# Optimization experiments

Hardware: AMD Instinct MI355X
Metric: run time of the kernel (lower is better)

The kernel has to match this reference:

```python
import jax, jax.numpy as jnp
import numpy as np

N = 50000   # n_nodes
E = 500000  # n_edges
D = 128     # input_dim == hidden_dim
L = 2       # n_layers
K = 5       # Chebyshev filter size


def setup_inputs() -> dict:
    key = jax.random.key(0)
    k0, k1, k2, k3, k4 = jax.random.split(key, 5)
    scale = 1.0 / np.sqrt(D)
    return {
        "edge_index": jax.random.randint(k0, (2, E), 0, N),
        "edge_weight": jax.random.uniform(k1, (E,), dtype=jnp.float32),
        "emb": jax.random.uniform(k2, (N, D), dtype=jnp.float32, minval=-1.0, maxval=1.0),
        "Wx": jax.random.normal(k3, (L, 3, K, D, D), dtype=jnp.float32) * scale,
        "bx": jnp.zeros((L, 3, D), dtype=jnp.float32),
        "Wh": jax.random.normal(k4, (L, 3, K, D, D), dtype=jnp.float32) * scale,
        "bh": jnp.zeros((L, 3, D), dtype=jnp.float32),
    }


def reference(edge_index, edge_weight, emb, Wx, bx, Wh, bh):
    src, dst = edge_index[0], edge_index[1]
    # ChebConv sym-normalized scaled Laplacian with lambda_max=2:
    # L_hat = L - I = -D^{-1/2} A D^{-1/2} (zero diagonal)
    deg = jax.ops.segment_sum(edge_weight, src, num_segments=N)
    dinv = jnp.where(deg > 0, deg ** -0.5, 0.0)
    w = -dinv[src] * edge_weight * dinv[dst]  # [E]

    def prop(x):  # L_hat @ x via gather/scatter over edges
        return jax.ops.segment_sum(w[:, None] * x[src], dst, num_segments=N)

    def cheb(x, W, b):  # sum_k T_k(L_hat) x W_k + b
        Tx0 = x
        out = Tx0 @ W[0]
        Tx1 = prop(Tx0)
        out = out + Tx1 @ W[1]
        for k in range(2, K):
            Tx2 = 2.0 * prop(Tx1) - Tx0
            out = out + Tx2 @ W[k]
            Tx0, Tx1 = Tx1, Tx2
        return out + b

    x = emb
    hidden_states = []
    for l in range(L):
        H = jnp.ones((N, D), x.dtype)  # init__hidd: ones
        Z = jax.nn.sigmoid(cheb(x, Wx[l, 0], bx[l, 0]) + cheb(H, Wh[l, 0], bh[l, 0]))
        R = jax.nn.sigmoid(cheb(x, Wx[l, 1], bx[l, 1]) + cheb(H, Wh[l, 1], bh[l, 1]))
        Ht = jnp.tanh(cheb(x, Wx[l, 2], bx[l, 2]) + cheb(H * R, Wh[l, 2], bh[l, 2]))
        Hn = Z * H + (1.0 - Z) * Ht
        h = jax.nn.relu(Hn)  # dropout is identity in eval mode
        hidden_states.append(h)
        x = h
    return x  # == hidden_states[-1]
```

## Files before the change

kernel.cpp:

```cpp
#include <hip/hip_runtime.h>
#include <math.h>

#define NN 50000
#define EE 500000
#define DD 128
#define KK 5
#define LL 2

typedef _Float16 f16x8 __attribute__((ext_vector_type(8)));
typedef float f32x4 __attribute__((ext_vector_type(4)));

__device__ __forceinline__ ushort f2h(float x) {
    union { _Float16 h; ushort u; } v; v.h = (_Float16)x; return v.u;
}


__global__ __launch_bounds__(256) void edge_pass1(
    const int* __restrict__ src, const int* __restrict__ dst,
    const float* __restrict__ ew,
    float* __restrict__ deg, int* __restrict__ hist)
{
    int e = blockIdx.x * blockDim.x + threadIdx.x;
    if (e >= EE) return;
    atomicAdd(&deg[src[e]], ew[e]);
    atomicAdd(&hist[dst[e]], 1);
}

__global__ __launch_bounds__(256) void dinv_kernel(
    const float* __restrict__ deg, float* __restrict__ dinv)
{
    int i = blockIdx.x * blockDim.x + threadIdx.x;
    if (i >= NN) return;
    float d = deg[i];
    dinv[i] = (d > 0.f) ? (1.f / sqrtf(d)) : 0.f;
}

#define SCAN_C ((NN + 1023) / 1024)
__global__ __launch_bounds__(1024) void scan_kernel(
    const int* __restrict__ hist, int* __restrict__ row_ptr)
{
    __shared__ int sums[1024];
    const int t = threadIdx.x;
    const int base = t * SCAN_C;
    int local[SCAN_C];
    int s = 0;
#pragma unroll
    for (int j = 0; j < SCAN_C; ++j) {
        int i = base + j;
        int v = (i < NN) ? hist[i] : 0;
        s += v;
        local[j] = s;
    }
    sums[t] = s;
    __syncthreads();
    for (int off = 1; off < 1024; off <<= 1) {
        int v = (t >= off) ? sums[t - off] : 0;
        __syncthreads();
        sums[t] += v;
        __syncthreads();
    }
    int excl = sums[t] - s;
    if (t == 0) row_ptr[0] = 0;
#pragma unroll
    for (int j = 0; j < SCAN_C; ++j) {
        int i = base + j;
        if (i < NN) row_ptr[i + 1] = excl + local[j];
    }
}

__global__ __launch_bounds__(256) void copy_fill(
    const int* __restrict__ row_ptr, int* __restrict__ fill)
{
    int i = blockIdx.x * blockDim.x + threadIdx.x;
    if (i < NN) fill[i] = row_ptr[i];
}

__global__ __launch_bounds__(256) void edge_scatter(
    const int* __restrict__ src, const int* __restrict__ dst,
    const float* __restrict__ ew, const float* __restrict__ dinv,
    int* __restrict__ fill,
    int* __restrict__ src_srt, float* __restrict__ w_srt)
{
    int e = blockIdx.x * blockDim.x + threadIdx.x;
    if (e >= EE) return;
    int s = src[e], t = dst[e];
    float w = -dinv[s] * ew[e] * dinv[t];
    int pos = atomicAdd(&fill[t], 1);
    src_srt[pos] = s;
    w_srt[pos] = w;
}

__global__ __launch_bounds__(256) void propv_kernel(
    const int* __restrict__ rp, const int* __restrict__ ss, const float* __restrict__ sw,
    const float* __restrict__ tin, const float* __restrict__ tprev, float* __restrict__ tout,
    float alpha, float beta, int ones_in, int ones_prev)
{
    int i = blockIdx.x * blockDim.x + threadIdx.x;
    if (i >= NN) return;
    float acc = 0.f;
    int e0 = rp[i], e1 = rp[i + 1];
    int e = e0;
    for (; e + 4 <= e1; e += 4) {
        float t0 = ones_in ? 1.f : tin[ss[e]];
        float t1v = ones_in ? 1.f : tin[ss[e + 1]];
        float t2v = ones_in ? 1.f : tin[ss[e + 2]];
        float t3v = ones_in ? 1.f : tin[ss[e + 3]];
        acc += sw[e] * t0 + sw[e + 1] * t1v + sw[e + 2] * t2v + sw[e + 3] * t3v;
    }
    for (; e < e1; ++e) {
        float tv = ones_in ? 1.f : tin[ss[e]];
        acc += sw[e] * tv;
    }
    float pv = ones_prev ? 1.f : (tprev ? tprev[i] : 0.f);
    tout[i] = alpha * acc + beta * pv;
}

__global__ __launch_bounds__(128) void colsum_kernel(
    const float* __restrict__ Wh, float* __restrict__ scol)
{
    int b = blockIdx.x;
    int k = b % KK;
    int g = (b / KK) % 2;
    int l = b / (2 * KK);
    int d = threadIdx.x;
    const float* Wp = Wh + ((size_t)((l * 3 + g) * KK + k)) * DD * DD;
    float s = 0.f;
    for (int r = 0; r < DD; ++r) s += Wp[r * DD + d];
    scol[((size_t)((l * 2 + g) * KK + k)) * DD + d] = s;
}

__global__ __launch_bounds__(256) void wconv_f16(
    const float* __restrict__ W, ushort* __restrict__ out, int mode)
{
    int t = blockIdx.x;
    int st = (mode == 0) ? t : ((t / KK) * 3 + 2) * KK + (t % KK);
    const float* Wp = W + (size_t)st * DD * DD;
    ushort* op = out + (size_t)t * DD * DD;
    for (int idx = threadIdx.x; idx < DD * DD; idx += 256) {
        int rb = idx >> 7, c = idx & 127;
        float w = Wp[c * DD + rb];
        int byte = rb * 256 + (((c * 2) ^ ((rb & 7) << 4)));
        *(ushort*)((char*)op + byte) = f2h(w);
    }
}

__global__ __launch_bounds__(256) void f32_to_f16(
    const float* __restrict__ in, ushort* __restrict__ out, int n8)
{
    int i = blockIdx.x * blockDim.x + threadIdx.x;
    if (i >= n8) return;
    float4 a = ((const float4*)in)[i * 2];
    float4 b = ((const float4*)in)[i * 2 + 1];
    f16x8 o;
    o[0] = (_Float16)a.x; o[1] = (_Float16)a.y; o[2] = (_Float16)a.z; o[3] = (_Float16)a.w;
    o[4] = (_Float16)b.x; o[5] = (_Float16)b.y; o[6] = (_Float16)b.z; o[7] = (_Float16)b.w;
    ((f16x8*)out)[i] = o;
}

__global__ __launch_bounds__(256) void prop_mat(
    const int* __restrict__ rp, const int* __restrict__ ss, const float* __restrict__ sw,
    const ushort* __restrict__ x, const ushort* __restrict__ prev,
    ushort* __restrict__ out, float alpha, float beta)
{
    int node = blockIdx.x * 16 + (threadIdx.x >> 4);
    if (node >= NN) return;
    int lane = threadIdx.x & 15;
    int c = lane * 8;
    float acc[8];
#pragma unroll
    for (int j = 0; j < 8; ++j) acc[j] = 0.f;
    int e0 = rp[node], e1 = rp[node + 1];
    int e = e0;
    for (; e + 4 <= e1; e += 4) {
        int s0 = ss[e], s1 = ss[e + 1], s2 = ss[e + 2], s3 = ss[e + 3];
        float w0 = sw[e], w1 = sw[e + 1], w2 = sw[e + 2], w3 = sw[e + 3];
        f16x8 r0 = *(const f16x8*)(x + (size_t)s0 * DD + c);
        f16x8 r1 = *(const f16x8*)(x + (size_t)s1 * DD + c);
        f16x8 r2 = *(const f16x8*)(x + (size_t)s2 * DD + c);
        f16x8 r3 = *(const f16x8*)(x + (size_t)s3 * DD + c);
#pragma unroll
        for (int j = 0; j < 8; ++j)
            acc[j] += w0 * (float)r0[j] + w1 * (float)r1[j] + w2 * (float)r2[j] + w3 * (float)r3[j];
    }
    for (; e < e1; ++e) {
        int s = ss[e];
        float w = sw[e];
        f16x8 r = *(const f16x8*)(x + (size_t)s * DD + c);
#pragma unroll
        for (int j = 0; j < 8; ++j) acc[j] += w * (float)r[j];
    }
    f16x8 o;
    if (beta != 0.f && prev) {
        f16x8 pv = *(const f16x8*)(prev + (size_t)node * DD + c);
#pragma unroll
        for (int j = 0; j < 8; ++j) o[j] = (_Float16)(alpha * acc[j] + beta * (float)pv[j]);
    } else {
#pragma unroll
        for (int j = 0; j < 8; ++j) o[j] = (_Float16)(alpha * acc[j]);
    }
    *(f16x8*)(out + (size_t)node * DD + c) = o;
}

__device__ __forceinline__ void mm_gate(
    const ushort* __restrict__ const* Ts, const ushort* __restrict__ Wg,
    ushort* Bs, int rowg0, int rowg1, bool ok0, bool ok1,
    int tid, int lk, f32x4 acc[2][8], int lr)
{
#pragma unroll
    for (int fr = 0; fr < 2; ++fr)
#pragma unroll
        for (int fc = 0; fc < 8; ++fc) acc[fr][fc] = (f32x4){0.f, 0.f, 0.f, 0.f};
#pragma unroll
    for (int k = 0; k < KK; ++k) {
        const ushort* Tk = Ts[k];
        const ushort* Bg = Wg + (size_t)k * (DD * DD);
        __syncthreads();
#pragma unroll
        for (int i = 0; i < 8; ++i) {
            int off = i * 4096 + tid * 16;
            uint4 v = *(const uint4*)((const char*)Bg + off);
            *(uint4*)((char*)Bs + off) = v;
        }
        f16x8 a[2][4];
#pragma unroll
        for (int fr = 0; fr < 2; ++fr) {
            int rowg = fr ? rowg1 : rowg0;
            bool ok = fr ? ok1 : ok0;
            const ushort* rp2 = Ts[k] + (size_t)rowg * DD + lk * 8;
            (void)Tk;
#pragma unroll
            for (int ko = 0; ko < 4; ++ko) {
                if (ok) a[fr][ko] = *(const f16x8*)(rp2 + ko * 32);
                else a[fr][ko] = (f16x8){0, 0, 0, 0, 0, 0, 0, 0};
            }
        }
        __syncthreads();
#pragma unroll
        for (int ko = 0; ko < 4; ++ko) {
            const int cb = ko * 64 + lk * 16;
#pragma unroll
            for (int fc = 0; fc < 8; ++fc) {
                int rb = fc * 16 + lr;
                int byte = (rb * 256 + cb) ^ ((rb & 7) << 4);
                f16x8 bfrag = *(const f16x8*)((const char*)Bs + byte);
                acc[0][fc] = __builtin_amdgcn_mfma_f32_16x16x32_f16(a[0][ko], bfrag, acc[0][fc], 0, 0, 0);
                acc[1][fc] = __builtin_amdgcn_mfma_f32_16x16x32_f16(a[1][ko], bfrag, acc[1][fc], 0, 0, 0);
            }
        }
    }
}

__device__ __forceinline__ int xcd_swz(int b, int nwg) {
    int xcd = b & 7, idx = b >> 3;
    int q = nwg >> 3, rr = nwg & 7;
    int start = (xcd < rr) ? xcd * (q + 1) : rr * (q + 1) + (xcd - rr) * q;
    return start + idx;
}

__global__ __launch_bounds__(256) void cheb_mm_zr(
    const ushort* __restrict__ T0, const ushort* __restrict__ T1,
    const ushort* __restrict__ T2, const ushort* __restrict__ T3,
    const ushort* __restrict__ T4,
    const ushort* __restrict__ Wt,
    const float* __restrict__ tvec, const float* __restrict__ scol,
    const float* __restrict__ bx, const float* __restrict__ bh, int l,
    float* __restrict__ Xz, ushort* __restrict__ Xr16, float* __restrict__ Xh)
{
    __shared__ ushort Bs[DD * DD];
    const int tile = xcd_swz(blockIdx.x, gridDim.x);
    const int tid = threadIdx.x;
    const int lane = tid & 63;
    const int wid = tid >> 6;
    const int lr = lane & 15;
    const int lk = lane >> 4;
    const int r0 = tile * 128;
    const ushort* Ts[5] = {T0, T1, T2, T3, T4};

    int rowg0 = r0 + wid * 32 + lr;
    int rowg1 = rowg0 + 16;
    bool ok0 = rowg0 < NN;
    bool ok1 = rowg1 < NN;

    f32x4 accZ[2][8], accB[2][8];
    mm_gate(Ts, Wt, Bs, rowg0, rowg1, ok0, ok1, tid, lk, accZ, lr);
    mm_gate(Ts, Wt + (size_t)KK * DD * DD, Bs, rowg0, rowg1, ok0, ok1, tid, lk, accB, lr);

    {
        const float* s0 = scol + (size_t)((l * 2 + 0) * KK) * DD;
        const float* s1 = scol + (size_t)((l * 2 + 1) * KK) * DD;
        const float* bz0 = bx + (size_t)(l * 3 + 0) * DD;
        const float* bz1 = bh + (size_t)(l * 3 + 0) * DD;
        const float* br0 = bx + (size_t)(l * 3 + 1) * DD;
        const float* br1 = bh + (size_t)(l * 3 + 1) * DD;
#pragma unroll
        for (int fr = 0; fr < 2; ++fr) {
#pragma unroll
            for (int j = 0; j < 4; ++j) {
                int grow = r0 + wid * 32 + fr * 16 + lk * 4 + j;
                if (grow < NN) {
                    float t1 = tvec[grow], t2 = tvec[NN + grow];
                    float t3 = tvec[2 * NN + grow], t4 = tvec[3 * NN + grow];
#pragma unroll
                    for (int fc = 0; fc < 8; ++fc) {
                        int d = fc * 16 + lr;
                        size_t idx = (size_t)grow * DD + d;
                        float hz = s0[d] + t1 * s0[DD + d] + t2 * s0[2 * DD + d]
                                 + t3 * s0[3 * DD + d] + t4 * s0[4 * DD + d];
                        float z = accZ[fr][fc][j] + bz0[d] + bz1[d] + hz;
                        z = 1.f / (1.f + expf(-z));
                        float hr = s1[d] + t1 * s1[DD + d] + t2 * s1[2 * DD + d]
                                 + t3 * s1[3 * DD + d] + t4 * s1[4 * DD + d];
                        float r = accB[fr][fc][j] + br0[d] + br1[d] + hr;
                        r = 1.f / (1.f + expf(-r));
                        Xz[idx] = z;
                        Xr16[idx] = f2h(r);
                    }
                }
            }
        }
    }

    mm_gate(Ts, Wt + (size_t)2 * KK * DD * DD, Bs, rowg0, rowg1, ok0, ok1, tid, lk, accZ, lr);
#pragma unroll
    for (int fr = 0; fr < 2; ++fr) {
#pragma unroll
        for (int j = 0; j < 4; ++j) {
            int grow = r0 + wid * 32 + fr * 16 + lk * 4 + j;
            if (grow < NN) {
#pragma unroll
                for (int fc = 0; fc < 8; ++fc) {
                    int d = fc * 16 + lr;
                    Xh[(size_t)grow * DD + d] = accZ[fr][fc][j];
                }
            }
        }
    }
}

__global__ __launch_bounds__(256) void cheb_mm_final(
    const ushort* __restrict__ T0, const ushort* __restrict__ T1,
    const ushort* __restrict__ T2, const ushort* __restrict__ T3,
    const ushort* __restrict__ T4,
    const ushort* __restrict__ Wt,
    const float* __restrict__ Xh, const float* __restrict__ Xz,
    const float* __restrict__ bx, const float* __restrict__ bh, int l,
    float* __restrict__ out, ushort* __restrict__ h16, int write_f32)
{
    __shared__ ushort Bs[DD * DD];
    const int tile = xcd_swz(blockIdx.x, gridDim.x);
    const int tid = threadIdx.x;
    const int lane = tid & 63;
    const int wid = tid >> 6;
    const int lr = lane & 15;
    const int lk = lane >> 4;
    const int r0 = tile * 128;
    const ushort* Ts[5] = {T0, T1, T2, T3, T4};

    int rowg0 = r0 + wid * 32 + lr;
    int rowg1 = rowg0 + 16;
    bool ok0 = rowg0 < NN;
    bool ok1 = rowg1 < NN;

    f32x4 acc[2][8];
    mm_gate(Ts, Wt, Bs, rowg0, rowg1, ok0, ok1, tid, lk, acc, lr);

    const float* b0 = bx + (size_t)(l * 3 + 2) * DD;
    const float* b1 = bh + (size_t)(l * 3 + 2) * DD;
#pragma unroll
    for (int fr = 0; fr < 2; ++fr) {
#pragma unroll
        for (int j = 0; j < 4; ++j) {
            int grow = r0 + wid * 32 + fr * 16 + lk * 4 + j;
            if (grow < NN) {
#pragma unroll
                for (int fc = 0; fc < 8; ++fc) {
                    int d = fc * 16 + lr;
                    size_t idx = (size_t)grow * DD + d;
                    float pre = acc[fr][fc][j] + Xh[idx] + b0[d] + b1[d];
                    float ht = tanhf(pre);
                    float z = Xz[idx];
                    float hn = z + (1.f - z) * ht;
                    float h = hn > 0.f ? hn : 0.f;
                    if (write_f32) out[idx] = h;
                    h16[idx] = f2h(h);
                }
            }
        }
    }
}


extern "C" void kernel_launch(void* const* d_in, const int* in_sizes, int n_in,
                              void* d_out, int out_size, void* d_ws, size_t ws_size,
                              hipStream_t stream)
{
    const int*   ei  = (const int*)d_in[0];
    const float* ew  = (const float*)d_in[1];
    const float* emb = (const float*)d_in[2];
    const float* Wx  = (const float*)d_in[3];
    const float* bx  = (const float*)d_in[4];
    const float* Wh  = (const float*)d_in[5];
    const float* bh  = (const float*)d_in[6];
    float* out = (float*)d_out;

    const int* src = ei;
    const int* dst = ei + EE;

    char* ws = (char*)d_ws;
    size_t off = 0;
    auto alloc = [&](size_t nbytes) -> char* {
        char* p = ws + off;
        off = (off + nbytes + 255) & ~(size_t)255;
        return p;
    };
    float*  deg     = (float*)alloc((size_t)NN * 4);
    float*  dinv    = (float*)alloc((size_t)NN * 4);
    int*    hist    = (int*)alloc((size_t)(NN + 1) * 4);
    int*    row_ptr = (int*)alloc((size_t)(NN + 1) * 4);
    int*    fill    = (int*)alloc((size_t)(NN + 1) * 4);
    int*    src_srt = (int*)alloc((size_t)EE * 4);
    float*  w_srt   = (float*)alloc((size_t)EE * 4);
    float*  tvec    = (float*)alloc((size_t)4 * NN * 4);
    float*  scol    = (float*)alloc((size_t)LL * 2 * KK * DD * 4);
    float*  Xz      = (float*)alloc((size_t)NN * DD * 4);
    float*  Xh      = (float*)alloc((size_t)NN * DD * 4);
    ushort* Th      = (ushort*)alloc((size_t)4 * NN * DD * 2);
    ushort* x_f16   = (ushort*)alloc((size_t)NN * DD * 2);
    ushort* Xr_f16  = (ushort*)alloc((size_t)NN * DD * 2);
    ushort* WxT     = (ushort*)alloc((size_t)LL * 3 * KK * DD * DD * 2);
    ushort* WhT2    = (ushort*)alloc((size_t)LL * KK * DD * DD * 2);
    (void)ws_size; (void)in_sizes; (void)n_in; (void)out_size;

    ushort* T1 = Th;
    ushort* T2 = Th + (size_t)NN * DD;
    ushort* T3 = Th + (size_t)2 * NN * DD;
    ushort* T4 = Th + (size_t)3 * NN * DD;

    const int EG = (EE + 255) / 256;
    const int NG = (NN + 255) / 256;
    const int PG = (NN + 15) / 16;
    const int MMG = (NN + 127) / 128;
    const int CVG = (NN * DD / 8 + 255) / 256;
    const int GATE_STRIDE = KK * DD * DD;

    hipMemsetAsync(deg, 0, (size_t)NN * 4, stream);
    hipMemsetAsync(hist, 0, (size_t)(NN + 1) * 4, stream);

    edge_pass1<<<EG, 256, 0, stream>>>(src, dst, ew, deg, hist);
    dinv_kernel<<<NG, 256, 0, stream>>>(deg, dinv);
    scan_kernel<<<1, 1024, 0, stream>>>(hist, row_ptr);
    copy_fill<<<NG, 256, 0, stream>>>(row_ptr, fill);
    edge_scatter<<<EG, 256, 0, stream>>>(src, dst, ew, dinv, fill, src_srt, w_srt);

    float* t1 = tvec;
    float* t2 = tvec + NN;
    float* t3 = tvec + 2 * NN;
    float* t4 = tvec + 3 * NN;
    propv_kernel<<<NG, 256, 0, stream>>>(row_ptr, src_srt, w_srt, nullptr, nullptr, t1, 1.f,  0.f, 1, 0);
    propv_kernel<<<NG, 256, 0, stream>>>(row_ptr, src_srt, w_srt, t1, nullptr,      t2, 2.f, -1.f, 0, 1);
    propv_kernel<<<NG, 256, 0, stream>>>(row_ptr, src_srt, w_srt, t2, t1,           t3, 2.f, -1.f, 0, 0);
    propv_kernel<<<NG, 256, 0, stream>>>(row_ptr, src_srt, w_srt, t3, t2,           t4, 2.f, -1.f, 0, 0);

    colsum_kernel<<<LL * 2 * KK, 128, 0, stream>>>(Wh, scol);

    wconv_f16<<<LL * 3 * KK, 256, 0, stream>>>(Wx, WxT, 0);
    wconv_f16<<<LL * KK, 256, 0, stream>>>(Wh, WhT2, 1);

    f32_to_f16<<<CVG, 256, 0, stream>>>(emb, x_f16, NN * DD / 8);

    for (int l = 0; l < LL; ++l) {
        prop_mat<<<PG, 256, 0, stream>>>(row_ptr, src_srt, w_srt, x_f16, nullptr, T1, 1.f,  0.f);
        prop_mat<<<PG, 256, 0, stream>>>(row_ptr, src_srt, w_srt, T1,    x_f16,   T2, 2.f, -1.f);
        prop_mat<<<PG, 256, 0, stream>>>(row_ptr, src_srt, w_srt, T2,    T1,      T3, 2.f, -1.f);
        prop_mat<<<PG, 256, 0, stream>>>(row_ptr, src_srt, w_srt, T3,    T2,      T4, 2.f, -1.f);

        cheb_mm_zr<<<MMG, 256, 0, stream>>>(x_f16, T1, T2, T3, T4,
                                            WxT + (size_t)l * 3 * GATE_STRIDE,
                                            tvec, scol, bx, bh, l,
                                            Xz, Xr_f16, Xh);

        prop_mat<<<PG, 256, 0, stream>>>(row_ptr, src_srt, w_srt, Xr_f16, nullptr, T1, 1.f,  0.f);
        prop_mat<<<PG, 256, 0, stream>>>(row_ptr, src_srt, w_srt, T1,     Xr_f16,  T2, 2.f, -1.f);
        prop_mat<<<PG, 256, 0, stream>>>(row_ptr, src_srt, w_srt, T2,     T1,      T3, 2.f, -1.f);
        prop_mat<<<PG, 256, 0, stream>>>(row_ptr, src_srt, w_srt, T3,     T2,      T4, 2.f, -1.f);

        cheb_mm_final<<<MMG, 256, 0, stream>>>(Xr_f16, T1, T2, T3, T4,
                                               WhT2 + (size_t)l * GATE_STRIDE,
                                               Xh, Xz, bx, bh, l,
                                               out, x_f16, (l == LL - 1) ? 1 : 0);
    }
}
```

Baseline: 957.5 us.

## Split gate matmuls across blocks, prelayout weights as MFMA fragments, widen gather unroll

The combined Z/R/H matmul kernel is split so each block computes one gate, tripling the grid. The final matmul uses 64-row tiles to launch more blocks. Weights are pre-laid out in MFMA fragment order, so the B operand becomes a single contiguous LDS read per lane instead of swizzled addressing. The sparse propagation gets an 8-way unrolled edge loop with nontemporal index and output accesses, and the last layer skips its redundant f16 store. In exchange, the T-matrix rows are reloaded once per gate, and each block now does less work per weight tile it stages.

Result: faster. 898.7 us (-6.1%).

```diff
diff --git a/kernel.cpp b/kernel.cpp
--- a/kernel.cpp
+++ b/kernel.cpp
@@ -9,6 +9,7 @@
 
 typedef _Float16 f16x8 __attribute__((ext_vector_type(8)));
 typedef float f32x4 __attribute__((ext_vector_type(4)));
+typedef unsigned int u32x4 __attribute__((ext_vector_type(4)));
 
 __device__ __forceinline__ ushort f2h(float x) {
     union { _Float16 h; ushort u; } v; v.h = (_Float16)x; return v.u;
@@ -129,7 +130,7 @@
     scol[((size_t)((l * 2 + g) * KK + k)) * DD + d] = s;
 }
 
-__global__ __launch_bounds__(256) void wconv_f16(
+__global__ __launch_bounds__(256) void wconv_frag(
     const float* __restrict__ W, ushort* __restrict__ out, int mode)
 {
     int t = blockIdx.x;
@@ -137,10 +138,14 @@
     const float* Wp = W + (size_t)st * DD * DD;
     ushort* op = out + (size_t)t * DD * DD;
     for (int idx = threadIdx.x; idx < DD * DD; idx += 256) {
-        int rb = idx >> 7, c = idx & 127;
-        float w = Wp[c * DD + rb];
-        int byte = rb * 256 + (((c * 2) ^ ((rb & 7) << 4)));
-        *(ushort*)((char*)op + byte) = f2h(w);
+        int j  = idx & 7;
+        int lr = (idx >> 3) & 15;
+        int lk = (idx >> 7) & 3;
+        int fc = (idx >> 9) & 7;
+        int ko = (idx >> 12) & 3;
+        int dout = fc * 16 + lr;
+        int din  = ko * 32 + lk * 8 + j;
+        op[idx] = f2h(Wp[din * DD + dout]);
     }
 }
 
@@ -171,6 +176,36 @@
     for (int j = 0; j < 8; ++j) acc[j] = 0.f;
     int e0 = rp[node], e1 = rp[node + 1];
     int e = e0;
+    for (; e + 8 <= e1; e += 8) {
+        int s0 = __builtin_nontemporal_load(ss + e);
+        int s1 = __builtin_nontemporal_load(ss + e + 1);
+        int s2 = __builtin_nontemporal_load(ss + e + 2);
+        int s3 = __builtin_nontemporal_load(ss + e + 3);
+        int s4 = __builtin_nontemporal_load(ss + e + 4);
+        int s5 = __builtin_nontemporal_load(ss + e + 5);
+        int s6 = __builtin_nontemporal_load(ss + e + 6);
+        int s7 = __builtin_nontemporal_load(ss + e + 7);
+        float w0 = __builtin_nontemporal_load(sw + e);
+        float w1 = __builtin_nontemporal_load(sw + e + 1);
+        float w2 = __builtin_nontemporal_load(sw + e + 2);
+        float w3 = __builtin_nontemporal_load(sw + e + 3);
+        float w4 = __builtin_nontemporal_load(sw + e + 4);
+        float w5 = __builtin_nontemporal_load(sw + e + 5);
+        float w6 = __builtin_nontemporal_load(sw + e + 6);
+        float w7 = __builtin_nontemporal_load(sw + e + 7);
+        f16x8 r0 = *(const f16x8*)(x + (size_t)s0 * DD + c);
+        f16x8 r1 = *(const f16x8*)(x + (size_t)s1 * DD + c);
+        f16x8 r2 = *(const f16x8*)(x + (size_t)s2 * DD + c);
+        f16x8 r3 = *(const f16x8*)(x + (size_t)s3 * DD + c);
+        f16x8 r4 = *(const f16x8*)(x + (size_t)s4 * DD + c);
+        f16x8 r5 = *(const f16x8*)(x + (size_t)s5 * DD + c);
+        f16x8 r6 = *(const f16x8*)(x + (size_t)s6 * DD + c);
+        f16x8 r7 = *(const f16x8*)(x + (size_t)s7 * DD + c);
+#pragma unroll
+        for (int j = 0; j < 8; ++j)
+            acc[j] += w0 * (float)r0[j] + w1 * (float)r1[j] + w2 * (float)r2[j] + w3 * (float)r3[j]
+                    + w4 * (float)r4[j] + w5 * (float)r5[j] + w6 * (float)r6[j] + w7 * (float)r7[j];
+    }
     for (; e + 4 <= e1; e += 4) {
         int s0 = ss[e], s1 = ss[e + 1], s2 = ss[e + 2], s3 = ss[e + 3];
         float w0 = sw[e], w1 = sw[e + 1], w2 = sw[e + 2], w3 = sw[e + 3];
@@ -189,30 +224,30 @@
 #pragma unroll
         for (int j = 0; j < 8; ++j) acc[j] += w * (float)r[j];
     }
-    f16x8 o;
+    union { f16x8 v; u32x4 u; } o;
     if (beta != 0.f && prev) {
         f16x8 pv = *(const f16x8*)(prev + (size_t)node * DD + c);
 #pragma unroll
-        for (int j = 0; j < 8; ++j) o[j] = (_Float16)(alpha * acc[j] + beta * (float)pv[j]);
+        for (int j = 0; j < 8; ++j) o.v[j] = (_Float16)(alpha * acc[j] + beta * (float)pv[j]);
     } else {
 #pragma unroll
-        for (int j = 0; j < 8; ++j) o[j] = (_Float16)(alpha * acc[j]);
-    }
-    *(f16x8*)(out + (size_t)node * DD + c) = o;
-}
-
+        for (int j = 0; j < 8; ++j) o.v[j] = (_Float16)(alpha * acc[j]);
+    }
+    __builtin_nontemporal_store(o.u, (u32x4*)(out + (size_t)node * DD + c));
+}
+
+template<int NFR>
 __device__ __forceinline__ void mm_gate(
     const ushort* __restrict__ const* Ts, const ushort* __restrict__ Wg,
-    ushort* Bs, int rowg0, int rowg1, bool ok0, bool ok1,
-    int tid, int lk, f32x4 acc[2][8], int lr)
-{
-#pragma unroll
-    for (int fr = 0; fr < 2; ++fr)
+    ushort* Bs, const int* rowg, const bool* ok,
+    int tid, int lane, int lk, f32x4 acc[NFR][8])
+{
+#pragma unroll
+    for (int fr = 0; fr < NFR; ++fr)
 #pragma unroll
         for (int fc = 0; fc < 8; ++fc) acc[fr][fc] = (f32x4){0.f, 0.f, 0.f, 0.f};
 #pragma unroll
     for (int k = 0; k < KK; ++k) {
-        const ushort* Tk = Ts[k];
         const ushort* Bg = Wg + (size_t)k * (DD * DD);
         __syncthreads();
 #pragma unroll
@@ -221,30 +256,25 @@
             uint4 v = *(const uint4*)((const char*)Bg + off);
             *(uint4*)((char*)Bs + off) = v;
         }
-        f16x8 a[2][4];
-#pragma unroll
-        for (int fr = 0; fr < 2; ++fr) {
-            int rowg = fr ? rowg1 : rowg0;
-            bool ok = fr ? ok1 : ok0;
-            const ushort* rp2 = Ts[k] + (size_t)rowg * DD + lk * 8;
-            (void)Tk;
+        f16x8 a[NFR][4];
+#pragma unroll
+        for (int fr = 0; fr < NFR; ++fr) {
+            const ushort* rp2 = Ts[k] + (size_t)rowg[fr] * DD + lk * 8;
 #pragma unroll
             for (int ko = 0; ko < 4; ++ko) {
-                if (ok) a[fr][ko] = *(const f16x8*)(rp2 + ko * 32);
+                if (ok[fr]) a[fr][ko] = *(const f16x8*)(rp2 + ko * 32);
                 else a[fr][ko] = (f16x8){0, 0, 0, 0, 0, 0, 0, 0};
             }
         }
         __syncthreads();
 #pragma unroll
         for (int ko = 0; ko < 4; ++ko) {
-            const int cb = ko * 64 + lk * 16;
 #pragma unroll
             for (int fc = 0; fc < 8; ++fc) {
-                int rb = fc * 16 + lr;
-                int byte = (rb * 256 + cb) ^ ((rb & 7) << 4);
-                f16x8 bfrag = *(const f16x8*)((const char*)Bs + byte);
-                acc[0][fc] = __builtin_amdgcn_mfma_f32_16x16x32_f16(a[0][ko], bfrag, acc[0][fc], 0, 0, 0);
-                acc[1][fc] = __builtin_amdgcn_mfma_f32_16x16x32_f16(a[1][ko], bfrag, acc[1][fc], 0, 0, 0);
+                f16x8 b = *(const f16x8*)(Bs + ko * 4096 + fc * 512 + lane * 8);
+#pragma unroll
+                for (int fr = 0; fr < NFR; ++fr)
+                    acc[fr][fc] = __builtin_amdgcn_mfma_f32_16x16x32_f16(a[fr][ko], b, acc[fr][fc], 0, 0, 0);
             }
         }
     }
@@ -261,13 +291,16 @@
     const ushort* __restrict__ T0, const ushort* __restrict__ T1,
     const ushort* __restrict__ T2, const ushort* __restrict__ T3,
     const ushort* __restrict__ T4,
-    const ushort* __restrict__ Wt,
+    const ushort* __restrict__ Wt, int gate_stride,
     const float* __restrict__ tvec, const float* __restrict__ scol,
     const float* __restrict__ bx, const float* __restrict__ bh, int l,
     float* __restrict__ Xz, ushort* __restrict__ Xr16, float* __restrict__ Xh)
 {
     __shared__ ushort Bs[DD * DD];
-    const int tile = xcd_swz(blockIdx.x, gridDim.x);
+    const int lin = xcd_swz(blockIdx.x, gridDim.x);
+    const int tile = lin / 3;
+    const int g = lin - tile * 3;
+
     const int tid = threadIdx.x;
     const int lane = tid & 63;
     const int wid = tid >> 6;
@@ -276,22 +309,29 @@
     const int r0 = tile * 128;
     const ushort* Ts[5] = {T0, T1, T2, T3, T4};
 
-    int rowg0 = r0 + wid * 32 + lr;
-    int rowg1 = rowg0 + 16;
-    bool ok0 = rowg0 < NN;
-    bool ok1 = rowg1 < NN;
-
-    f32x4 accZ[2][8], accB[2][8];
-    mm_gate(Ts, Wt, Bs, rowg0, rowg1, ok0, ok1, tid, lk, accZ, lr);
-    mm_gate(Ts, Wt + (size_t)KK * DD * DD, Bs, rowg0, rowg1, ok0, ok1, tid, lk, accB, lr);
-
-    {
-        const float* s0 = scol + (size_t)((l * 2 + 0) * KK) * DD;
-        const float* s1 = scol + (size_t)((l * 2 + 1) * KK) * DD;
-        const float* bz0 = bx + (size_t)(l * 3 + 0) * DD;
-        const float* bz1 = bh + (size_t)(l * 3 + 0) * DD;
-        const float* br0 = bx + (size_t)(l * 3 + 1) * DD;
-        const float* br1 = bh + (size_t)(l * 3 + 1) * DD;
+    int rowg[2] = {r0 + wid * 32 + lr, r0 + wid * 32 + lr + 16};
+    bool ok[2] = {rowg[0] < NN, rowg[1] < NN};
+
+    f32x4 acc[2][8];
+    mm_gate<2>(Ts, Wt + (size_t)g * gate_stride, Bs, rowg, ok, tid, lane, lk, acc);
+
+    if (g == 2) {
+#pragma unroll
+        for (int fr = 0; fr < 2; ++fr) {
+#pragma unroll
+            for (int j = 0; j < 4; ++j) {
+                int grow = r0 + wid * 32 + fr * 16 + lk * 4 + j;
+                if (grow < NN) {
+#pragma unroll
+                    for (int fc = 0; fc < 8; ++fc)
+                        Xh[(size_t)grow * DD + fc * 16 + lr] = acc[fr][fc][j];
+                }
+            }
+        }
+    } else {
+        const float* sc = scol + (size_t)((l * 2 + g) * KK) * DD;
+        const float* b0 = bx + (size_t)(l * 3 + g) * DD;
+        const float* b1 = bh + (size_t)(l * 3 + g) * DD;
 #pragma unroll
         for (int fr = 0; fr < 2; ++fr) {
 #pragma unroll
@@ -304,33 +344,13 @@
                     for (int fc = 0; fc < 8; ++fc) {
                         int d = fc * 16 + lr;
                         size_t idx = (size_t)grow * DD + d;
-                        float hz = s0[d] + t1 * s0[DD + d] + t2 * s0[2 * DD + d]
-                                 + t3 * s0[3 * DD + d] + t4 * s0[4 * DD + d];
-                        float z = accZ[fr][fc][j] + bz0[d] + bz1[d] + hz;
-                        z = 1.f / (1.f + expf(-z));
-                        float hr = s1[d] + t1 * s1[DD + d] + t2 * s1[2 * DD + d]
-                                 + t3 * s1[3 * DD + d] + t4 * s1[4 * DD + d];
-                        float r = accB[fr][fc][j] + br0[d] + br1[d] + hr;
-                        r = 1.f / (1.f + expf(-r));
-                        Xz[idx] = z;
-                        Xr16[idx] = f2h(r);
+                        float hh = sc[d] + t1 * sc[DD + d] + t2 * sc[2 * DD + d]
+                                 + t3 * sc[3 * DD + d] + t4 * sc[4 * DD + d];
+                        float v = acc[fr][fc][j] + b0[d] + b1[d] + hh;
+                        v = 1.f / (1.f + expf(-v));
+                        if (g == 0) Xz[idx] = v;
+                        else Xr16[idx] = f2h(v);
                     }
-                }
-            }
-        }
-    }
-
-    mm_gate(Ts, Wt + (size_t)2 * KK * DD * DD, Bs, rowg0, rowg1, ok0, ok1, tid, lk, accZ, lr);
-#pragma unroll
-    for (int fr = 0; fr < 2; ++fr) {
-#pragma unroll
-        for (int j = 0; j < 4; ++j) {
-            int grow = r0 + wid * 32 + fr * 16 + lk * 4 + j;
-            if (grow < NN) {
-#pragma unroll
-                for (int fc = 0; fc < 8; ++fc) {
-                    int d = fc * 16 + lr;
-                    Xh[(size_t)grow * DD + d] = accZ[fr][fc][j];
                 }
             }
         }
@@ -353,37 +373,32 @@
     const int wid = tid >> 6;
     const int lr = lane & 15;
     const int lk = lane >> 4;
-    const int r0 = tile * 128;
+    const int r0 = tile * 64;
     const ushort* Ts[5] = {T0, T1, T2, T3, T4};
 
-    int rowg0 = r0 + wid * 32 + lr;
-    int rowg1 = rowg0 + 16;
-    bool ok0 = rowg0 < NN;
-    bool ok1 = rowg1 < NN;
-
-    f32x4 acc[2][8];
-    mm_gate(Ts, Wt, Bs, rowg0, rowg1, ok0, ok1, tid, lk, acc, lr);
+    int rowg[1] = {r0 + wid * 16 + lr};
+    bool ok[1] = {rowg[0] < NN};
+
+    f32x4 acc[1][8];
+    mm_gate<1>(Ts, Wt, Bs, rowg, ok, tid, lane, lk, acc);
 
     const float* b0 = bx + (size_t)(l * 3 + 2) * DD;
     const float* b1 = bh + (size_t)(l * 3 + 2) * DD;
 #pragma unroll
-    for (int fr = 0; fr < 2; ++fr) {
-#pragma unroll
-        for (int j = 0; j < 4; ++j) {
-            int grow = r0 + wid * 32 + fr * 16 + lk * 4 + j;
-            if (grow < NN) {
-#pragma unroll
-                for (int fc = 0; fc < 8; ++fc) {
-                    int d = fc * 16 + lr;
-                    size_t idx = (size_t)grow * DD + d;
-                    float pre = acc[fr][fc][j] + Xh[idx] + b0[d] + b1[d];
-                    float ht = tanhf(pre);
-                    float z = Xz[idx];
-                    float hn = z + (1.f - z) * ht;
-                    float h = hn > 0.f ? hn : 0.f;
-                    if (write_f32) out[idx] = h;
-                    h16[idx] = f2h(h);
-                }
+    for (int j = 0; j < 4; ++j) {
+        int grow = r0 + wid * 16 + lk * 4 + j;
+        if (grow < NN) {
+#pragma unroll
+            for (int fc = 0; fc < 8; ++fc) {
+                int d = fc * 16 + lr;
+                size_t idx = (size_t)grow * DD + d;
+                float pre = acc[0][fc][j] + Xh[idx] + b0[d] + b1[d];
+                float ht = tanhf(pre);
+                float z = Xz[idx];
+                float hn = z + (1.f - z) * ht;
+                float h = hn > 0.f ? hn : 0.f;
+                if (write_f32) out[idx] = h;
+                else h16[idx] = f2h(h);
             }
         }
     }
@@ -440,6 +455,7 @@
     const int NG = (NN + 255) / 256;
     const int PG = (NN + 15) / 16;
     const int MMG = (NN + 127) / 128;
+    const int MMG2 = (NN + 63) / 64;
     const int CVG = (NN * DD / 8 + 255) / 256;
     const int GATE_STRIDE = KK * DD * DD;
 
@@ -463,8 +479,8 @@
 
     colsum_kernel<<<LL * 2 * KK, 128, 0, stream>>>(Wh, scol);
 
-    wconv_f16<<<LL * 3 * KK, 256, 0, stream>>>(Wx, WxT, 0);
-    wconv_f16<<<LL * KK, 256, 0, stream>>>(Wh, WhT2, 1);
+    wconv_frag<<<LL * 3 * KK, 256, 0, stream>>>(Wx, WxT, 0);
+    wconv_frag<<<LL * KK, 256, 0, stream>>>(Wh, WhT2, 1);
 
     f32_to_f16<<<CVG, 256, 0, stream>>>(emb, x_f16, NN * DD / 8);
 
@@ -474,17 +490,17 @@
         prop_mat<<<PG, 256, 0, stream>>>(row_ptr, src_srt, w_srt, T2,    T1,      T3, 2.f, -1.f);
         prop_mat<<<PG, 256, 0, stream>>>(row_ptr, src_srt, w_srt, T3,    T2,      T4, 2.f, -1.f);
 
-        cheb_mm_zr<<<MMG, 256, 0, stream>>>(x_f16, T1, T2, T3, T4,
-                                            WxT + (size_t)l * 3 * GATE_STRIDE,
-                                            tvec, scol, bx, bh, l,
-                                            Xz, Xr_f16, Xh);
+        cheb_mm_zr<<<MMG * 3, 256, 0, stream>>>(x_f16, T1, T2, T3, T4,
+                                             WxT + (size_t)l * 3 * GATE_STRIDE, GATE_STRIDE,
+                                             tvec, scol, bx, bh, l,
+                                             Xz, Xr_f16, Xh);
 
         prop_mat<<<PG, 256, 0, stream>>>(row_ptr, src_srt, w_srt, Xr_f16, nullptr, T1, 1.f,  0.f);
         prop_mat<<<PG, 256, 0, stream>>>(row_ptr, src_srt, w_srt, T1,     Xr_f16,  T2, 2.f, -1.f);
         prop_mat<<<PG, 256, 0, stream>>>(row_ptr, src_srt, w_srt, T2,     T1,      T3, 2.f, -1.f);
         prop_mat<<<PG, 256, 0, stream>>>(row_ptr, src_srt, w_srt, T3,     T2,      T4, 2.f, -1.f);
 
-        cheb_mm_final<<<MMG, 256, 0, stream>>>(Xr_f16, T1, T2, T3, T4,
+        cheb_mm_final<<<MMG2, 256, 0, stream>>>(Xr_f16, T1, T2, T3, T4,
                                                WhT2 + (size_t)l * GATE_STRIDE,
                                                Xh, Xz, bx, bh, l,
                                                out, x_f16, (l == LL - 1) ? 1 : 0);
```
